# Kernel optimization log

Measured on AMD Instinct MI355X. Metric: run time of the kernel, lower is better.

## Reference

```python
import jax, jax.numpy as jnp
import numpy as np
from jax.scipy.special import logsumexp


def _lstm(x, mask, Wk, Wr, b, reverse=False):
    # x: [B,T,D], mask: [B,T] bool. Keras LSTM defaults: gate order i,f,g,o,
    # sigmoid recurrent activation, tanh activation. Masked steps carry state.
    if reverse:
        x = x[:, ::-1]
        mask = mask[:, ::-1]
    B, T, _ = x.shape
    H = Wr.shape[0]
    xz = jnp.einsum('btd,dh->bth', x, Wk) + b  # [B,T,4H] input projections, done once

    def step(carry, inp):
        h, c = carry
        z_t, m = inp  # [B,4H], [B]
        z = z_t + h @ Wr
        i, f, g, o = jnp.split(z, 4, axis=-1)
        i = jax.nn.sigmoid(i)
        f = jax.nn.sigmoid(f)
        g = jnp.tanh(g)
        o = jax.nn.sigmoid(o)
        c_new = f * c + i * g
        h_new = o * jnp.tanh(c_new)
        m = m[:, None]
        h = jnp.where(m, h_new, h)
        c = jnp.where(m, c_new, c)
        return (h, c), h

    h0 = jnp.zeros((B, H), x.dtype)
    (_, _), hs = jax.lax.scan(step, (h0, h0), (xz.transpose(1, 0, 2), mask.T))
    hs = hs.transpose(1, 0, 2)  # [B,T,H]
    if reverse:
        hs = hs[:, ::-1]
    return hs


def _crf_log_likelihood(logits, tags, lengths, trans):
    # TFA crf_log_likelihood: sequence_score - log_norm (forward algorithm)
    B, T, C = logits.shape
    t_idx = jnp.arange(T)
    mask = t_idx[None, :] < lengths[:, None]  # [B,T]
    # unary score: sum_t logits[b,t,tags[b,t]] over valid t
    unary = jnp.take_along_axis(logits, tags[..., None], axis=2)[..., 0]
    unary = jnp.sum(jnp.where(mask, unary, 0.0), axis=1)
    # binary score: sum_t trans[tags[t], tags[t+1]] for t < len-1
    binary = trans[tags[:, :-1], tags[:, 1:]]  # [B,T-1]
    mask2 = t_idx[None, : T - 1] < (lengths - 1)[:, None]
    binary = jnp.sum(jnp.where(mask2, binary, 0.0), axis=1)
    # log normalizer via forward algorithm scan
    alpha0 = logits[:, 0]  # [B,C]

    def step(alpha, inp):
        logit_t, m = inp  # [B,C], [B]
        new = logsumexp(alpha[:, :, None] + trans[None], axis=1) + logit_t
        alpha = jnp.where(m[:, None], new, alpha)
        return alpha, None

    alpha, _ = jax.lax.scan(step, alpha0,
                            (logits[:, 1:].transpose(1, 0, 2), mask[:, 1:].T))
    log_norm = logsumexp(alpha, axis=1)
    return unary + binary - log_norm


def setup_inputs() -> dict:
    key = jax.random.key(0)
    ks = jax.random.split(key, 12)
    V, D, H, C, B, T = 30000, 300, 256, 9, 64, 512
    lengths = jax.random.randint(ks[0], (B,), T // 4, T + 1).astype(jnp.int32)
    valid = jnp.arange(T)[None, :] < lengths[:, None]
    inputs = (jax.random.randint(ks[1], (B, T), 1, V) * valid).astype(jnp.int32)
    targets = (jax.random.randint(ks[2], (B, T), 0, C) * valid).astype(jnp.int32)
    s = 0.05
    return {
        'inputs': inputs,
        'inputs_length': lengths,
        'targets': targets,
        'embedding': jax.random.normal(ks[3], (V, D), jnp.float32) * s,
        'Wk_f': jax.random.normal(ks[4], (D, 4 * H), jnp.float32) * s,
        'Wr_f': jax.random.normal(ks[5], (H, 4 * H), jnp.float32) * s,
        'b_f': jnp.zeros((4 * H,), jnp.float32),
        'Wk_b': jax.random.normal(ks[6], (D, 4 * H), jnp.float32) * s,
        'Wr_b': jax.random.normal(ks[7], (H, 4 * H), jnp.float32) * s,
        'b_b': jnp.zeros((4 * H,), jnp.float32),
        'dense_W': jax.random.normal(ks[8], (2 * H, C), jnp.float32) * s,
        'dense_b': jnp.zeros((C,), jnp.float32),
        'trans': jax.random.uniform(ks[9], (C, C), jnp.float32),
    }


def reference(inputs, inputs_length, targets, embedding, Wk_f, Wr_f, b_f,
              Wk_b, Wr_b, b_b, dense_W, dense_b, trans):
    T = inputs.shape[1]
    mask = jnp.arange(T)[None, :] < inputs_length[:, None]  # [B,T]
    emb = embedding[inputs]  # [B,T,D] (dropout is identity in inference)
    h_f = _lstm(emb, mask, Wk_f, Wr_f, b_f, reverse=False)
    h_b = _lstm(emb, mask, Wk_b, Wr_b, b_b, reverse=True)
    h = jnp.concatenate([h_f, h_b], axis=-1)  # [B,T,2H]
    logits = h @ dense_W + dense_b  # [B,T,C]
    log_likelihood = _crf_log_likelihood(logits, targets, inputs_length, trans)
    return logits, log_likelihood, trans
```

## Files before the change

kernel.cpp:

```cpp
#include <hip/hip_runtime.h>
#include <cstdint>
#include <cstddef>

typedef unsigned int  u32;
typedef unsigned short u16;
typedef _Float16 f16;
typedef _Float16 f16x2 __attribute__((ext_vector_type(2)));
typedef _Float16 half8 __attribute__((ext_vector_type(8)));
typedef float    f32x4v __attribute__((ext_vector_type(4)));
typedef int      i32x4 __attribute__((ext_vector_type(4)));

#define BATCH 64
#define TSEQ  512
#define DEMB  300
#define KPAD  320
#define HDIM  256
#define G4    1024
#define NCLS  9

__device__ __forceinline__ u32 packf16(float a, float b) {
  f16x2 v; v.x = (f16)a; v.y = (f16)b;
  return __builtin_bit_cast(u32, v);
}
__device__ __forceinline__ float f16f(u16 x) {
  return (float)__builtin_bit_cast(f16, x);
}
__device__ __forceinline__ float sigm_fast(float x) {
  return __builtin_amdgcn_rcpf(1.f + __expf(-x));
}
__device__ __forceinline__ float tanh_fast(float x) {
  float ax = __builtin_fabsf(x);
  float e = __expf(-2.f * ax);
  float t = (1.f - e) * __builtin_amdgcn_rcpf(1.f + e);
  return copysignf(t, x);
}

__global__ __launch_bounds__(256) void embcvt_k(const float* __restrict__ emb,
                                                u16* __restrict__ out) {
  const int v  = blockIdx.x * 16 + (threadIdx.x >> 4);
  const int kc = threadIdx.x & 15;
  u32* __restrict__ dst = (u32*)(out + (size_t)v * KPAD + kc * 20);
  if (kc < 15) {
    const float* __restrict__ src = emb + (size_t)v * DEMB + kc * 20;
    float tmp[20];
#pragma unroll
    for (int j = 0; j < 20; ++j) tmp[j] = src[j];
#pragma unroll
    for (int j = 0; j < 10; ++j) dst[j] = packf16(tmp[2 * j], tmp[2 * j + 1]);
  } else {
#pragma unroll
    for (int j = 0; j < 10; ++j) dst[j] = 0u;
  }
}

__global__ __launch_bounds__(256) void wkt_k(const float* __restrict__ Wk_f,
                                             const float* __restrict__ Wk_b,
                                             u16* __restrict__ wkt) {
  const int dir = blockIdx.y;
  const float* __restrict__ Wk = dir ? Wk_b : Wk_f;
  const int col = blockIdx.x * 16 + (threadIdx.x >> 4);
  const int kc  = threadIdx.x & 15;
  u32* __restrict__ dst = (u32*)(wkt + ((size_t)dir * G4 + col) * KPAD + kc * 20);
  if (kc < 15) {
    float tmp[20];
#pragma unroll
    for (int j = 0; j < 20; ++j) tmp[j] = Wk[(size_t)(kc * 20 + j) * G4 + col];
#pragma unroll
    for (int j = 0; j < 10; ++j) dst[j] = packf16(tmp[2 * j], tmp[2 * j + 1]);
  } else {
#pragma unroll
    for (int j = 0; j < 10; ++j) dst[j] = 0u;
  }
}

__global__ __launch_bounds__(256) void wr8_k(const float* __restrict__ Wr_f,
                                             const float* __restrict__ Wr_b,
                                             signed char* __restrict__ wr8) {
  const int dir = blockIdx.y;
  const float* __restrict__ Wr = dir ? Wr_b : Wr_f;
  const int col = blockIdx.x * 16 + (threadIdx.x >> 4);
  const int k0  = (threadIdx.x & 15) * 16;
  float tmp[16];
#pragma unroll
  for (int j = 0; j < 16; ++j) tmp[j] = Wr[(size_t)(k0 + j) * G4 + col];
  u32 pw[4];
#pragma unroll
  for (int jj = 0; jj < 4; ++jj) {
    u32 p = 0;
#pragma unroll
    for (int b = 0; b < 4; ++b) {
      int q = (int)__builtin_rintf(tmp[4 * jj + b] * 512.f);
      q = q > 127 ? 127 : (q < -127 ? -127 : q);
      p |= ((u32)(q & 255)) << (8 * b);
    }
    pw[jj] = p;
  }
  *(uint4*)(wr8 + ((size_t)dir * G4 + col) * HDIM + k0) =
      make_uint4(pw[0], pw[1], pw[2], pw[3]);
}

__global__ __launch_bounds__(256) void xz_gemm_k(
    const int* __restrict__ inputs, const u16* __restrict__ wkt,
    const u16* __restrict__ embf16, const float* __restrict__ b_f,
    const float* __restrict__ b_b, u16* __restrict__ xz)
{
  __shared__ __align__(16) u16 As[128 * 40];
  __shared__ __align__(16) u16 Bs[128 * 40];
  const int tid  = threadIdx.x;
  const int wv   = tid >> 6, lane = tid & 63;
  const int quad = lane >> 4, fl = lane & 15;
  const int cbi  = blockIdx.x;
  const int dir  = cbi >> 3;
  const int cb1  = (cbi & 7) * 128;
  const int rb   = blockIdx.y * 128;
  const float* __restrict__ bias = dir ? b_b : b_f;

  const int sm = tid >> 1, sh = (tid & 1) * 16;
  const int vrow = inputs[rb + sm];
  const u16* __restrict__ asrc = wkt + ((size_t)(dir * G4) + cb1 + sm) * KPAD + sh;
  const u16* __restrict__ bsrc = embf16 + (size_t)vrow * KPAD + sh;

  f32x4v acc[2][8];
#pragma unroll
  for (int bt = 0; bt < 2; ++bt)
#pragma unroll
    for (int i = 0; i < 8; ++i) acc[bt][i] = (f32x4v){0.f, 0.f, 0.f, 0.f};

  for (int kt = 0; kt < 10; ++kt) {
    const int k0 = kt * 32;
    uint4 a0v = *(const uint4*)(asrc + k0);
    uint4 a1v = *(const uint4*)(asrc + k0 + 8);
    uint4 b0v = *(const uint4*)(bsrc + k0);
    uint4 b1v = *(const uint4*)(bsrc + k0 + 8);
    *(uint4*)&As[sm * 40 + sh]     = a0v;
    *(uint4*)&As[sm * 40 + sh + 8] = a1v;
    *(uint4*)&Bs[sm * 40 + sh]     = b0v;
    *(uint4*)&Bs[sm * 40 + sh + 8] = b1v;
    __syncthreads();
    half8 bf[2];
#pragma unroll
    for (int bt = 0; bt < 2; ++bt)
      bf[bt] = *(const half8*)&Bs[(wv * 32 + bt * 16 + fl) * 40 + quad * 8];
#pragma unroll
    for (int i = 0; i < 8; ++i) {
      half8 af = *(const half8*)&As[(i * 16 + fl) * 40 + quad * 8];
      acc[0][i] = __builtin_amdgcn_mfma_f32_16x16x32_f16(af, bf[0], acc[0][i], 0, 0, 0);
      acc[1][i] = __builtin_amdgcn_mfma_f32_16x16x32_f16(af, bf[1], acc[1][i], 0, 0, 0);
    }
    __syncthreads();
  }
#pragma unroll
  for (int bt = 0; bt < 2; ++bt) {
    const int row = rb + wv * 32 + bt * 16 + fl;
    u16* __restrict__ orow = xz + ((size_t)(dir * BATCH * TSEQ) + row) * G4;
#pragma unroll
    for (int i = 0; i < 8; ++i) {
      const int mb = cb1 + i * 16 + quad * 4;
      const float4 bb = *(const float4*)&bias[mb];
      f32x4v v = acc[bt][i];
      uint2 pk;
      pk.x = packf16(v[0] + bb.x, v[1] + bb.y);
      pk.y = packf16(v[2] + bb.z, v[3] + bb.w);
      *(uint2*)&orow[mb] = pk;
    }
  }
}

#define MFI(a, b, c) __builtin_amdgcn_mfma_i32_16x16x64_i8(a, b, c, 0, 0, 0)
#define LD8(g, ct, kc) (*(const i32x4*)(wr8w + (size_t)((g) * 256 + 32 * w + (ct) * 16 + l15) * HDIM + (kc) * 64 + q16))
#define DECL8(g, ct) \
  i32x4 W##g##ct##_0 = LD8(g, ct, 0), W##g##ct##_1 = LD8(g, ct, 1), \
        W##g##ct##_2 = LD8(g, ct, 2), W##g##ct##_3 = LD8(g, ct, 3); \
  asm volatile("" : "+a"(W##g##ct##_0), "+a"(W##g##ct##_1), \
                    "+a"(W##g##ct##_2), "+a"(W##g##ct##_3));
#define TILE(g, ct) \
  i32x4 ac##g##ct = (i32x4){0, 0, 0, 0}; \
  ac##g##ct = MFI(af0, W##g##ct##_0, ac##g##ct); \
  ac##g##ct = MFI(af1, W##g##ct##_1, ac##g##ct); \
  ac##g##ct = MFI(af2, W##g##ct##_2, ac##g##ct); \
  ac##g##ct = MFI(af3, W##g##ct##_3, ac##g##ct);

__global__ __launch_bounds__(512, 2) void lstm_k(
    const u16* __restrict__ xz, const signed char* __restrict__ wr8,
    const int* __restrict__ lengths, u16* __restrict__ hcat)
{
  const int chain = blockIdx.x;
  const int dir   = chain >> 6;
  const int batch = chain & 63;
  const int tid  = threadIdx.x;
  const int w    = tid >> 6;
  const int lane = tid & 63;
  const int quad = lane >> 4, l15 = lane & 15;
  const int q16  = quad * 16;
  const int ctsel = quad & 1;
  const int j    = 32 * w + ctsel * 16 + l15;
  const int wr   = quad < 2;
  const float DEQ = 1.f / (512.f * 127.f);

  __shared__ __align__(16) signed char hpk[2][256];

  const signed char* __restrict__ wr8w = wr8 + (size_t)dir * G4 * HDIM;

  DECL8(0, 0) DECL8(0, 1) DECL8(1, 0) DECL8(1, 1)
  DECL8(2, 0) DECL8(2, 1) DECL8(3, 0) DECL8(3, 1)

  if (tid < 256) hpk[0][tid] = 0;

  float c = 0.f, h = 0.f;
  const int len = lengths[batch];
  const u16* __restrict__ xzb = xz + (size_t)(dir * BATCH + batch) * TSEQ * G4;
  u16* __restrict__ hrow = hcat + (size_t)batch * TSEQ * 512 + dir * 256;
  __syncthreads();

  int tt = dir ? (TSEQ - 1) : 0;
  const int dt = dir ? -1 : 1;
  u16 x0 = xzb[(size_t)tt * G4 + j];
  u16 x1 = xzb[(size_t)tt * G4 + 256 + j];
  u16 x2 = xzb[(size_t)tt * G4 + 512 + j];
  u16 x3 = xzb[(size_t)tt * G4 + 768 + j];

  for (int st = 0; st < TSEQ; ++st) {
    const int ttn = (st == TSEQ - 1) ? tt : tt + dt;
    u16 xn0 = xzb[(size_t)ttn * G4 + j];
    u16 xn1 = xzb[(size_t)ttn * G4 + 256 + j];
    u16 xn2 = xzb[(size_t)ttn * G4 + 512 + j];
    u16 xn3 = xzb[(size_t)ttn * G4 + 768 + j];

    const int par = st & 1;
    const signed char* hb = &hpk[par][0];
    i32x4 af0 = *(const i32x4*)(hb + q16);
    i32x4 af1 = *(const i32x4*)(hb + 64 + q16);
    i32x4 af2 = *(const i32x4*)(hb + 128 + q16);
    i32x4 af3 = *(const i32x4*)(hb + 192 + q16);

    TILE(0, 0) TILE(0, 1)
    TILE(1, 0) TILE(1, 1)
    TILE(2, 0) TILE(2, 1)
    TILE(3, 0) TILE(3, 1)

    int ri = ctsel ? ac01[0] : ac00[0];
    int rf = ctsel ? ac11[0] : ac10[0];
    int rg = ctsel ? ac21[0] : ac20[0];
    int ro = ctsel ? ac31[0] : ac30[0];

    float zi = (float)ri * DEQ + f16f(x0);
    float zf = (float)rf * DEQ + f16f(x1);
    float zg = (float)rg * DEQ + f16f(x2);
    float zo = (float)ro * DEQ + f16f(x3);
    float ig = sigm_fast(zi);
    float fg = sigm_fast(zf);
    float gg = tanh_fast(zg);
    float og = sigm_fast(zo);
    float cn = fg * c + ig * gg;
    float hn = og * tanh_fast(cn);
    if (tt < len) { c = cn; h = hn; }
    if (wr) {
      u32 hb2 = packf16(h, h);
      hrow[(size_t)tt * 512 + j] = (u16)(hb2 & 0xffffu);
      int hq = (int)__builtin_rintf(h * 127.f);
      hpk[par ^ 1][j] = (signed char)hq;
    }
    __syncthreads();
    x0 = xn0; x1 = xn1; x2 = xn2; x3 = xn3; tt = ttn;
  }
}

__global__ __launch_bounds__(256) void dense_k(
    const u16* __restrict__ hcat, const float* __restrict__ W,
    const float* __restrict__ bias, float* __restrict__ out)
{
  const int lane = threadIdx.x & 63;
  const int wv = threadIdx.x >> 6;
  const int rowbase = (blockIdx.x * 4 + wv) * 8;
  for (int rr = 0; rr < 8; ++rr) {
    const int row = rowbase + rr;
    const u16* __restrict__ hr = hcat + (size_t)row * 512;
    float hv[8];
#pragma unroll
    for (int i = 0; i < 8; ++i)
      hv[i] = f16f(hr[i * 64 + lane]);
    float myout = 0.f;
#pragma unroll
    for (int cc = 0; cc < 9; ++cc) {
      float p = 0.f;
#pragma unroll
      for (int i = 0; i < 8; ++i)
        p = fmaf(hv[i], W[(size_t)(i * 64 + lane) * 9 + cc], p);
#pragma unroll
      for (int o = 32; o > 0; o >>= 1) p += __shfl_xor(p, o);
      if (lane == cc) myout = p + bias[cc];
    }
    if (lane < 9) out[(size_t)row * 9 + lane] = myout;
  }
}

__global__ __launch_bounds__(64) void crf_k(
    const float* __restrict__ logits, const int* __restrict__ tags,
    const int* __restrict__ lengths, const float* __restrict__ trans,
    float* __restrict__ out_ll, float* __restrict__ out_trans)
{
  const int b = blockIdx.x;
  const int lane = threadIdx.x;
  const int len = lengths[b];
  const float* __restrict__ lg = logits + (size_t)b * TSEQ * NCLS;
  const int* __restrict__ tg = tags + (size_t)b * TSEQ;

  float ua = 0.f, ba = 0.f;
  for (int t = lane; t < TSEQ; t += 64) {
    int tag = tg[t];
    if (t < len) ua += lg[t * 9 + tag];
    if (t < len - 1) ba += trans[tag * 9 + tg[t + 1]];
  }
  float s = ua + ba;
#pragma unroll
  for (int o = 32; o > 0; o >>= 1) s += __shfl_xor(s, o);

  const int j = (lane < 9) ? lane : 0;
  float trc[9], alpha[9];
#pragma unroll
  for (int i = 0; i < 9; ++i) trc[i] = trans[i * 9 + j];
#pragma unroll
  for (int i = 0; i < 9; ++i) alpha[i] = lg[i];
  for (int t = 1; t < TSEQ; ++t) {
    if (t >= len) break;
    float m = -1e30f;
#pragma unroll
    for (int i = 0; i < 9; ++i) m = fmaxf(m, alpha[i] + trc[i]);
    float ss = 0.f;
#pragma unroll
    for (int i = 0; i < 9; ++i) ss += __expf(alpha[i] + trc[i] - m);
    float nj = __logf(ss) + m + lg[t * 9 + j];
#pragma unroll
    for (int i = 0; i < 9; ++i) alpha[i] = __shfl(nj, i);
  }
  float m2 = -1e30f;
#pragma unroll
  for (int i = 0; i < 9; ++i) m2 = fmaxf(m2, alpha[i]);
  float s2 = 0.f;
#pragma unroll
  for (int i = 0; i < 9; ++i) s2 += __expf(alpha[i] - m2);
  float lse = __logf(s2) + m2;
  if (lane == 0) out_ll[b] = s - lse;
  if (b == 0)
    for (int i = lane; i < 81; i += 64) out_trans[i] = trans[i];
}

extern "C" void kernel_launch(void* const* d_in, const int* in_sizes, int n_in,
                              void* d_out, int out_size, void* d_ws, size_t ws_size,
                              hipStream_t stream)
{
  const int*   inputs  = (const int*)d_in[0];
  const int*   lengths = (const int*)d_in[1];
  const int*   targets = (const int*)d_in[2];
  const float* emb     = (const float*)d_in[3];
  const float* Wk_f    = (const float*)d_in[4];
  const float* Wr_f    = (const float*)d_in[5];
  const float* b_f     = (const float*)d_in[6];
  const float* Wk_b    = (const float*)d_in[7];
  const float* Wr_b    = (const float*)d_in[8];
  const float* b_b     = (const float*)d_in[9];
  const float* dense_W = (const float*)d_in[10];
  const float* dense_b = (const float*)d_in[11];
  const float* trans   = (const float*)d_in[12];

  char* ws = (char*)d_ws;
  u16*         wkt    = (u16*)ws;
  signed char* wr8    = (signed char*)(ws + 1310720ull);
  u16*         embf16 = (u16*)(ws + 1835008ull);
  u16*         xz     = (u16*)(ws + 1835008ull + 19200000ull);
  u16*         hcat   = (u16*)(ws + 1835008ull + 19200000ull + 134217728ull);

  float* out_logits = (float*)d_out;
  float* out_ll     = out_logits + (size_t)BATCH * TSEQ * NCLS;
  float* out_trans  = out_ll + BATCH;

  hipLaunchKernelGGL(embcvt_k, dim3(1875), dim3(256), 0, stream, emb, embf16);
  hipLaunchKernelGGL(wkt_k, dim3(64, 2), dim3(256), 0, stream, Wk_f, Wk_b, wkt);
  hipLaunchKernelGGL(wr8_k, dim3(64, 2), dim3(256), 0, stream, Wr_f, Wr_b, wr8);
  hipLaunchKernelGGL(xz_gemm_k, dim3(16, 256), dim3(256), 0, stream,
                     inputs, wkt, embf16, b_f, b_b, xz);
  hipLaunchKernelGGL(lstm_k, dim3(128), dim3(512), 0, stream,
                     xz, wr8, lengths, hcat);
  hipLaunchKernelGGL(dense_k, dim3(1024), dim3(256), 0, stream,
                     hcat, dense_W, dense_b, out_logits);
  hipLaunchKernelGGL(crf_k, dim3(64), dim3(64), 0, stream,
                     out_logits, targets, lengths, trans, out_ll, out_trans);
}
```

Before: 722.0 us.

## Merge prep kernels and restructure input GEMM to stage embedding rows once

Merges the embedding, Wk and Wr conversion kernels into a single launch, and vectorises the embedding reads as float4. Rewrites the input-projection GEMM so each block loads its 64 gathered embedding rows into shared memory once, covering the full K. It then loops over all 16 column blocks of both directions, reading the weight fragments straight from global memory. This removes repeated embedding gathers, per-k-tile barriers and two launches, but it relies on cache hits for the weight reads and raises register pressure.

```diff
diff --git a/kernel.cpp b/kernel.cpp
--- a/kernel.cpp
+++ b/kernel.cpp
@@ -35,133 +35,154 @@
   return copysignf(t, x);
 }
 
-__global__ __launch_bounds__(256) void embcvt_k(const float* __restrict__ emb,
-                                                u16* __restrict__ out) {
-  const int v  = blockIdx.x * 16 + (threadIdx.x >> 4);
-  const int kc = threadIdx.x & 15;
-  u32* __restrict__ dst = (u32*)(out + (size_t)v * KPAD + kc * 20);
-  if (kc < 15) {
-    const float* __restrict__ src = emb + (size_t)v * DEMB + kc * 20;
-    float tmp[20];
-#pragma unroll
-    for (int j = 0; j < 20; ++j) tmp[j] = src[j];
-#pragma unroll
-    for (int j = 0; j < 10; ++j) dst[j] = packf16(tmp[2 * j], tmp[2 * j + 1]);
-  } else {
-#pragma unroll
-    for (int j = 0; j < 10; ++j) dst[j] = 0u;
-  }
-}
-
-__global__ __launch_bounds__(256) void wkt_k(const float* __restrict__ Wk_f,
-                                             const float* __restrict__ Wk_b,
-                                             u16* __restrict__ wkt) {
-  const int dir = blockIdx.y;
-  const float* __restrict__ Wk = dir ? Wk_b : Wk_f;
-  const int col = blockIdx.x * 16 + (threadIdx.x >> 4);
-  const int kc  = threadIdx.x & 15;
-  u32* __restrict__ dst = (u32*)(wkt + ((size_t)dir * G4 + col) * KPAD + kc * 20);
-  if (kc < 15) {
-    float tmp[20];
-#pragma unroll
-    for (int j = 0; j < 20; ++j) tmp[j] = Wk[(size_t)(kc * 20 + j) * G4 + col];
-#pragma unroll
-    for (int j = 0; j < 10; ++j) dst[j] = packf16(tmp[2 * j], tmp[2 * j + 1]);
-  } else {
-#pragma unroll
-    for (int j = 0; j < 10; ++j) dst[j] = 0u;
-  }
-}
-
-__global__ __launch_bounds__(256) void wr8_k(const float* __restrict__ Wr_f,
-                                             const float* __restrict__ Wr_b,
-                                             signed char* __restrict__ wr8) {
-  const int dir = blockIdx.y;
-  const float* __restrict__ Wr = dir ? Wr_b : Wr_f;
-  const int col = blockIdx.x * 16 + (threadIdx.x >> 4);
-  const int k0  = (threadIdx.x & 15) * 16;
-  float tmp[16];
-#pragma unroll
-  for (int j = 0; j < 16; ++j) tmp[j] = Wr[(size_t)(k0 + j) * G4 + col];
-  u32 pw[4];
-#pragma unroll
-  for (int jj = 0; jj < 4; ++jj) {
-    u32 p = 0;
-#pragma unroll
-    for (int b = 0; b < 4; ++b) {
-      int q = (int)__builtin_rintf(tmp[4 * jj + b] * 512.f);
-      q = q > 127 ? 127 : (q < -127 ? -127 : q);
-      p |= ((u32)(q & 255)) << (8 * b);
-    }
-    pw[jj] = p;
-  }
-  *(uint4*)(wr8 + ((size_t)dir * G4 + col) * HDIM + k0) =
-      make_uint4(pw[0], pw[1], pw[2], pw[3]);
-}
-
-__global__ __launch_bounds__(256) void xz_gemm_k(
+__global__ __launch_bounds__(256) void prep_k(
+    const float* __restrict__ emb, u16* __restrict__ embf16,
+    const float* __restrict__ Wk_f, const float* __restrict__ Wk_b,
+    u16* __restrict__ wkt,
+    const float* __restrict__ Wr_f, const float* __restrict__ Wr_b,
+    signed char* __restrict__ wr8)
+{
+  const int bid = blockIdx.x;
+  if (bid < 1875) {
+    const int v  = bid * 16 + (threadIdx.x >> 4);
+    const int kc = threadIdx.x & 15;
+    uint2* __restrict__ dst = (uint2*)(embf16 + (size_t)v * KPAD + kc * 20);
+    if (kc < 15) {
+      const float4* __restrict__ src =
+          (const float4*)(emb + (size_t)v * DEMB + kc * 20);
+      float4 t0 = src[0], t1 = src[1], t2 = src[2], t3 = src[3], t4 = src[4];
+      dst[0] = make_uint2(packf16(t0.x, t0.y), packf16(t0.z, t0.w));
+      dst[1] = make_uint2(packf16(t1.x, t1.y), packf16(t1.z, t1.w));
+      dst[2] = make_uint2(packf16(t2.x, t2.y), packf16(t2.z, t2.w));
+      dst[3] = make_uint2(packf16(t3.x, t3.y), packf16(t3.z, t3.w));
+      dst[4] = make_uint2(packf16(t4.x, t4.y), packf16(t4.z, t4.w));
+    } else {
+#pragma unroll
+      for (int j = 0; j < 5; ++j) dst[j] = make_uint2(0u, 0u);
+    }
+    return;
+  }
+  const int t   = bid - 1875;
+  const int dir = t >> 6;
+  const int blk = t & 63;
+  {
+    const float* __restrict__ Wk = dir ? Wk_b : Wk_f;
+    const int col = blk * 16 + (threadIdx.x >> 4);
+    const int kc  = threadIdx.x & 15;
+    u32* __restrict__ dst = (u32*)(wkt + ((size_t)dir * G4 + col) * KPAD + kc * 20);
+    if (kc < 15) {
+      float tmp[20];
+#pragma unroll
+      for (int j = 0; j < 20; ++j) tmp[j] = Wk[(size_t)(kc * 20 + j) * G4 + col];
+#pragma unroll
+      for (int j = 0; j < 10; ++j) dst[j] = packf16(tmp[2 * j], tmp[2 * j + 1]);
+    } else {
+#pragma unroll
+      for (int j = 0; j < 10; ++j) dst[j] = 0u;
+    }
+  }
+  {
+    const float* __restrict__ Wr = dir ? Wr_b : Wr_f;
+    const int col = blk * 16 + (threadIdx.x >> 4);
+    const int k0  = (threadIdx.x & 15) * 16;
+    float tmp[16];
+#pragma unroll
+    for (int j = 0; j < 16; ++j) tmp[j] = Wr[(size_t)(k0 + j) * G4 + col];
+    u32 pw[4];
+#pragma unroll
+    for (int jj = 0; jj < 4; ++jj) {
+      u32 p = 0;
+#pragma unroll
+      for (int b = 0; b < 4; ++b) {
+        int q = (int)__builtin_rintf(tmp[4 * jj + b] * 512.f);
+        q = q > 127 ? 127 : (q < -127 ? -127 : q);
+        p |= ((u32)(q & 255)) << (8 * b);
+      }
+      pw[jj] = p;
+    }
+    *(uint4*)(wr8 + ((size_t)dir * G4 + col) * HDIM + k0) =
+        make_uint4(pw[0], pw[1], pw[2], pw[3]);
+  }
+}
+
+__global__ __launch_bounds__(256, 2) void xz_gemm_k(
     const int* __restrict__ inputs, const u16* __restrict__ wkt,
     const u16* __restrict__ embf16, const float* __restrict__ b_f,
     const float* __restrict__ b_b, u16* __restrict__ xz)
 {
-  __shared__ __align__(16) u16 As[128 * 40];
-  __shared__ __align__(16) u16 Bs[128 * 40];
+  __shared__ __align__(16) u16 Bs[64 * 328];
   const int tid  = threadIdx.x;
   const int wv   = tid >> 6, lane = tid & 63;
   const int quad = lane >> 4, fl = lane & 15;
-  const int cbi  = blockIdx.x;
-  const int dir  = cbi >> 3;
-  const int cb1  = (cbi & 7) * 128;
-  const int rb   = blockIdx.y * 128;
-  const float* __restrict__ bias = dir ? b_b : b_f;
-
-  const int sm = tid >> 1, sh = (tid & 1) * 16;
-  const int vrow = inputs[rb + sm];
-  const u16* __restrict__ asrc = wkt + ((size_t)(dir * G4) + cb1 + sm) * KPAD + sh;
-  const u16* __restrict__ bsrc = embf16 + (size_t)vrow * KPAD + sh;
-
-  f32x4v acc[2][8];
-#pragma unroll
-  for (int bt = 0; bt < 2; ++bt)
-#pragma unroll
-    for (int i = 0; i < 8; ++i) acc[bt][i] = (f32x4v){0.f, 0.f, 0.f, 0.f};
-
-  for (int kt = 0; kt < 10; ++kt) {
-    const int k0 = kt * 32;
-    uint4 a0v = *(const uint4*)(asrc + k0);
-    uint4 a1v = *(const uint4*)(asrc + k0 + 8);
-    uint4 b0v = *(const uint4*)(bsrc + k0);
-    uint4 b1v = *(const uint4*)(bsrc + k0 + 8);
-    *(uint4*)&As[sm * 40 + sh]     = a0v;
-    *(uint4*)&As[sm * 40 + sh + 8] = a1v;
-    *(uint4*)&Bs[sm * 40 + sh]     = b0v;
-    *(uint4*)&Bs[sm * 40 + sh + 8] = b1v;
-    __syncthreads();
-    half8 bf[2];
-#pragma unroll
-    for (int bt = 0; bt < 2; ++bt)
-      bf[bt] = *(const half8*)&Bs[(wv * 32 + bt * 16 + fl) * 40 + quad * 8];
-#pragma unroll
-    for (int i = 0; i < 8; ++i) {
-      half8 af = *(const half8*)&As[(i * 16 + fl) * 40 + quad * 8];
-      acc[0][i] = __builtin_amdgcn_mfma_f32_16x16x32_f16(af, bf[0], acc[0][i], 0, 0, 0);
-      acc[1][i] = __builtin_amdgcn_mfma_f32_16x16x32_f16(af, bf[1], acc[1][i], 0, 0, 0);
-    }
-    __syncthreads();
-  }
-#pragma unroll
-  for (int bt = 0; bt < 2; ++bt) {
-    const int row = rb + wv * 32 + bt * 16 + fl;
-    u16* __restrict__ orow = xz + ((size_t)(dir * BATCH * TSEQ) + row) * G4;
-#pragma unroll
-    for (int i = 0; i < 8; ++i) {
-      const int mb = cb1 + i * 16 + quad * 4;
-      const float4 bb = *(const float4*)&bias[mb];
-      f32x4v v = acc[bt][i];
-      uint2 pk;
-      pk.x = packf16(v[0] + bb.x, v[1] + bb.y);
-      pk.y = packf16(v[2] + bb.z, v[3] + bb.w);
-      *(uint2*)&orow[mb] = pk;
+  const int rb   = blockIdx.x * 64;
+
+  {
+    const int srow = tid >> 2, seg = (tid & 3) * 80;
+    const int vrow = inputs[rb + srow];
+    const u16* __restrict__ bsrc = embf16 + (size_t)vrow * KPAD + seg;
+#pragma unroll
+    for (int jj = 0; jj < 10; ++jj) {
+      uint4 v = *(const uint4*)(bsrc + jj * 8);
+      *(uint4*)&Bs[srow * 328 + seg + jj * 8] = v;
+    }
+  }
+  __syncthreads();
+
+#pragma unroll
+  for (int grp = 0; grp < 4; ++grp) {
+    f32x4v acc[4][2][4];
+#pragma unroll
+    for (int d = 0; d < 4; ++d)
+#pragma unroll
+      for (int i = 0; i < 2; ++i)
+#pragma unroll
+        for (int bt = 0; bt < 4; ++bt) acc[d][i][bt] = (f32x4v){0.f, 0.f, 0.f, 0.f};
+
+#pragma unroll
+    for (int kt = 0; kt < 10; ++kt) {
+      half8 bf[4];
+#pragma unroll
+      for (int bt = 0; bt < 4; ++bt)
+        bf[bt] = *(const half8*)&Bs[(bt * 16 + fl) * 328 + kt * 32 + quad * 8];
+#pragma unroll
+      for (int d = 0; d < 4; ++d) {
+        const int dcb = grp * 4 + d;
+        const int dir = dcb >> 3;
+        const int cb1 = (dcb & 7) * 128;
+        const u16* __restrict__ arow =
+            wkt + ((size_t)(dir * G4) + cb1 + wv * 32 + fl) * KPAD + quad * 8;
+#pragma unroll
+        for (int i = 0; i < 2; ++i) {
+          half8 af = *(const half8*)(arow + (size_t)(i * 16) * KPAD + kt * 32);
+#pragma unroll
+          for (int bt = 0; bt < 4; ++bt)
+            acc[d][i][bt] = __builtin_amdgcn_mfma_f32_16x16x32_f16(
+                af, bf[bt], acc[d][i][bt], 0, 0, 0);
+        }
+      }
+    }
+
+#pragma unroll
+    for (int d = 0; d < 4; ++d) {
+      const int dcb = grp * 4 + d;
+      const int dir = dcb >> 3;
+      const int cb1 = (dcb & 7) * 128;
+      const float* __restrict__ bias = dir ? b_b : b_f;
+#pragma unroll
+      for (int bt = 0; bt < 4; ++bt) {
+        const int row = rb + bt * 16 + fl;
+        u16* __restrict__ orow = xz + ((size_t)(dir * BATCH * TSEQ) + row) * G4;
+#pragma unroll
+        for (int i = 0; i < 2; ++i) {
+          const int mb = cb1 + wv * 32 + i * 16 + quad * 4;
+          const float4 bb = *(const float4*)&bias[mb];
+          f32x4v v = acc[d][i][bt];
+          uint2 pk;
+          pk.x = packf16(v[0] + bb.x, v[1] + bb.y);
+          pk.y = packf16(v[2] + bb.z, v[3] + bb.w);
+          *(uint2*)&orow[mb] = pk;
+        }
+      }
     }
   }
 }
@@ -374,10 +395,9 @@
   float* out_ll     = out_logits + (size_t)BATCH * TSEQ * NCLS;
   float* out_trans  = out_ll + BATCH;
 
-  hipLaunchKernelGGL(embcvt_k, dim3(1875), dim3(256), 0, stream, emb, embf16);
-  hipLaunchKernelGGL(wkt_k, dim3(64, 2), dim3(256), 0, stream, Wk_f, Wk_b, wkt);
-  hipLaunchKernelGGL(wr8_k, dim3(64, 2), dim3(256), 0, stream, Wr_f, Wr_b, wr8);
-  hipLaunchKernelGGL(xz_gemm_k, dim3(16, 256), dim3(256), 0, stream,
+  hipLaunchKernelGGL(prep_k, dim3(2003), dim3(256), 0, stream,
+                     emb, embf16, Wk_f, Wk_b, wkt, Wr_f, Wr_b, wr8);
+  hipLaunchKernelGGL(xz_gemm_k, dim3(512), dim3(256), 0, stream,
                      inputs, wkt, embf16, b_f, b_b, xz);
   hipLaunchKernelGGL(lstm_k, dim3(128), dim3(512), 0, stream,
                      xz, wr8, lengths, hcat);
```

After: 745.0 us. +3.2%, slower.
